# Kernel optimization log

Measured on AMD Instinct MI355X. Metric: run time of the kernel, lower is better.

## Reference

```python
import jax, jax.numpy as jnp
import numpy as np

BB_MIN = -2.0
BB_MAX = 2.0
GRID_RES = 256
VOXEL_SIZE = (BB_MAX - BB_MIN) / (GRID_RES - 1)
# corner order matches torch code x1..x8: (dx,dy,dz) with dx outer, dz inner
CORNERS = [(dx, dy, dz) for dx in (0, 1) for dy in (0, 1) for dz in (0, 1)]


def _grid_normals(g, vs):
    # central differences interior, one-sided extrapolated boundary (as in get_grid_normal)
    def axis_normal(ax):
        n = g.shape[ax] - 1
        sl = lambda a, b: jax.lax.slice_in_dim(g, a, b, axis=ax)
        hi = (3 * sl(n, n + 1) - sl(n - 2, n - 1)) / 2
        lo = (3 * sl(0, 1) - sl(2, 3)) / 2
        fwd = jnp.concatenate([sl(1, n + 1), hi], axis=ax)
        bwd = jnp.concatenate([lo, sl(0, n)], axis=ax)
        return (fwd - bwd) / (2 * vs)
    return axis_normal(0), axis_normal(1), axis_normal(2)


def _gather8(gn, x, y, z):
    # flat index = z + R*y + R*R*x, 8 voxel corners -> [H, W, 8]
    flat = gn.reshape(-1)
    idx = jnp.stack([(z + dz) + GRID_RES * (y + dy) + GRID_RES * GRID_RES * (x + dx)
                     for dx, dy, dz in CORNERS], axis=-1)
    return jnp.take(flat, idx)


def _trilinear(c, tx, ty, tz):
    # weight order matches get_intersection_normal
    w = jnp.stack([
        (1 - tz) * (1 - ty) * (1 - tx), tz * (1 - ty) * (1 - tx),
        (1 - tz) * ty * (1 - tx),       tz * ty * (1 - tx),
        (1 - tz) * (1 - ty) * tx,       tz * (1 - ty) * tx,
        (1 - tz) * ty * tx,             tz * ty * tx], axis=-1)
    return jnp.sum(c * w, axis=-1)


def setup_inputs() -> dict:
    key = jax.random.key(0)
    k0, k1, k2, k3 = jax.random.split(key, 4)
    H, W = 400, 3200
    grid = jax.random.normal(k0, (GRID_RES, GRID_RES, GRID_RES), dtype=jnp.float32) * 0.1
    voxel_idx = jax.random.randint(k1, (H, W, 3), 0, GRID_RES - 1)  # <=254, +1 stays in-range
    voxel_min_point = BB_MIN + voxel_idx.astype(jnp.float32) * VOXEL_SIZE
    intersection_pos = voxel_min_point + jax.random.uniform(k2, (H, W, 3), dtype=jnp.float32) * VOXEL_SIZE
    mask = jax.random.randint(k3, (H, W), 0, 2)
    return {"grid": grid, "voxel_idx": voxel_idx, "intersection_pos": intersection_pos,
            "voxel_min_point": voxel_min_point, "mask": mask}


def reference(grid, voxel_idx, intersection_pos, voxel_min_point, mask):
    nx, ny, nz = _grid_normals(grid, VOXEL_SIZE)
    x = voxel_idx[..., 0]
    y = voxel_idx[..., 1]
    z = voxel_idx[..., 2]
    m = mask.astype(grid.dtype)
    t = (intersection_pos - voxel_min_point) / VOXEL_SIZE
    tx, ty, tz = t[..., 0], t[..., 1], t[..., 2]
    inv = (1 - m)[..., None]  # masked-out rays get +1 on all 8 corners (as in source)
    normals = jnp.stack([
        _trilinear(_gather8(gn, x, y, z) + inv, tx, ty, tz)
        for gn in (nx, ny, nz)], axis=-1)  # [H, W, 3]
    # relu(-grid) value gather at the base corner, zeroed where mask==0
    gridx = jnp.take(jax.nn.relu(-grid).reshape(-1),
                     z + GRID_RES * y + GRID_RES * GRID_RES * x) * m
    return jnp.concatenate([normals, gridx[..., None]], axis=-1)  # [H, W, 4]
```

## Files before the change

kernel.cpp:

```cpp
#include <hip/hip_runtime.h>
#include <hip/hip_bf16.h>

#define GRID_R   256
#define GRID_RR  65536
#define NVOX     16777216
#define NBRK     128
#define INV_2VS  31.875f
#define INV_VS   63.75f
#define VSF      0.015686275f

__device__ __forceinline__ float h2f(unsigned short u) {
    union { unsigned short s; _Float16 f; } cv; cv.s = u; return (float)cv.f;
}
__device__ __forceinline__ unsigned f2h2(float a, float b) {
    union { unsigned short s; _Float16 f; } ca, cb;
    ca.f = (_Float16)a; cb.f = (_Float16)b;
    return (unsigned)ca.s | ((unsigned)cb.s << 16);
}


__global__ __launch_bounds__(256) void precompute_brick_kernel(
    const float* __restrict__ grid,
    uint2*       __restrict__ packed)
{
    int bid = blockIdx.x;
    int t   = threadIdx.x;
    int xcd = bid & 7;
    int idx = bid >> 3;
    int bxl = idx >> 6;
    int byp = idx & 63;
    int bx  = (xcd << 4) + bxl;
    int by  = (byp << 1) + (t >> 7);
    int bz  = t & 127;

    int x0 = bx << 1, y0 = by << 1, z0 = bz << 1;
    int x1 = x0 + 1, y1 = y0 + 1, z1 = z0 + 1;

    int xm = (x0 == 0) ? 0 : x0 - 1;          int xp = (x1 == 255) ? 255 : x1 + 1;
    int ym = (y0 == 0) ? 0 : y0 - 1;          int yp = (y1 == 255) ? 255 : y1 + 1;
    int zm = (z0 == 0) ? 0 : z0 - 1;          int zp = (z1 == 255) ? 255 : z1 + 1;

    #define G2(X,Y,Z) (*reinterpret_cast<const float2*>(grid + (((X)*GRID_R + (Y)) << 8) + (Z)))
    #define G1(X,Y,Z) (grid[(((X)*GRID_R + (Y)) << 8) + (Z)])

    float2 c00 = G2(x0, y0, z0), c01 = G2(x0, y1, z0);
    float2 c10 = G2(x1, y0, z0), c11 = G2(x1, y1, z0);
    float c[2][2][2] = {{{c00.x, c00.y}, {c01.x, c01.y}},
                        {{c10.x, c10.y}, {c11.x, c11.y}}};

    float2 xl0 = G2(xm, y0, z0), xl1 = G2(xm, y1, z0);
    float2 xh0 = G2(xp, y0, z0), xh1 = G2(xp, y1, z0);
    float xlo[2][2] = {{xl0.x, xl0.y}, {xl1.x, xl1.y}};
    float xhi[2][2] = {{xh0.x, xh0.y}, {xh1.x, xh1.y}};

    float2 yl0 = G2(x0, ym, z0), yl1 = G2(x1, ym, z0);
    float2 yh0 = G2(x0, yp, z0), yh1 = G2(x1, yp, z0);
    float ylo[2][2] = {{yl0.x, yl0.y}, {yl1.x, yl1.y}};
    float yhi[2][2] = {{yh0.x, yh0.y}, {yh1.x, yh1.y}};

    float zlo[2][2], zhi[2][2];
    zlo[0][0] = G1(x0, y0, zm); zlo[0][1] = G1(x0, y1, zm);
    zlo[1][0] = G1(x1, y0, zm); zlo[1][1] = G1(x1, y1, zm);
    zhi[0][0] = G1(x0, y0, zp); zhi[0][1] = G1(x0, y1, zp);
    zhi[1][0] = G1(x1, y0, zp); zhi[1][1] = G1(x1, y1, zp);
    #undef G2
    #undef G1

    bool xb0 = (x0 == 0), xb1 = (x1 == 255);
    bool yb0 = (y0 == 0), yb1 = (y1 == 255);
    bool zb0 = (z0 == 0), zb1 = (z1 == 255);

    uint2 slot[8];
    #pragma unroll
    for (int dx = 0; dx < 2; ++dx)
    #pragma unroll
    for (int dy = 0; dy < 2; ++dy)
    #pragma unroll
    for (int dz = 0; dz < 2; ++dz) {
        float g0 = c[dx][dy][dz];

        float nx;
        if (xb0 && dx == 0)      nx = (c[1][dy][dz] - 1.5f*g0 + 0.5f*xhi[dy][dz]) * INV_2VS;
        else if (xb1 && dx == 1) nx = (1.5f*g0 - 0.5f*xlo[dy][dz] - c[0][dy][dz]) * INV_2VS;
        else nx = ((dx ? xhi[dy][dz] : c[1][dy][dz]) - (dx ? c[0][dy][dz] : xlo[dy][dz])) * INV_2VS;

        float ny;
        if (yb0 && dy == 0)      ny = (c[dx][1][dz] - 1.5f*g0 + 0.5f*yhi[dx][dz]) * INV_2VS;
        else if (yb1 && dy == 1) ny = (1.5f*g0 - 0.5f*ylo[dx][dz] - c[dx][0][dz]) * INV_2VS;
        else ny = ((dy ? yhi[dx][dz] : c[dx][1][dz]) - (dy ? c[dx][0][dz] : ylo[dx][dz])) * INV_2VS;

        float nz;
        if (zb0 && dz == 0)      nz = (c[dx][dy][1] - 1.5f*g0 + 0.5f*zhi[dx][dy]) * INV_2VS;
        else if (zb1 && dz == 1) nz = (1.5f*g0 - 0.5f*zlo[dx][dy] - c[dx][dy][0]) * INV_2VS;
        else nz = ((dz ? zhi[dx][dy] : c[dx][dy][1]) - (dz ? c[dx][dy][0] : zlo[dx][dy])) * INV_2VS;

        int s = dx*4 + dy*2 + dz;
        slot[s].x = f2h2(nx, ny);
        slot[s].y = f2h2(nz, g0);
    }

    long long B = ((long long)(bx*NBRK + by))*NBRK + bz;
    uint4* dst = reinterpret_cast<uint4*>(packed) + B*4;
    #pragma unroll
    for (int j = 0; j < 4; ++j) {
        uint4 st; st.x = slot[2*j].x; st.y = slot[2*j].y;
                  st.z = slot[2*j+1].x; st.w = slot[2*j+1].y;
        dst[j] = st;
    }
}

__global__ __launch_bounds__(256) void gather_kernel(
    const uint2* __restrict__ packed,
    const int*   __restrict__ vidx,
    const float* __restrict__ ipos,
    const int*   __restrict__ mask,
    float*       __restrict__ out,
    int n)
{
    int i = blockIdx.x * blockDim.x + threadIdx.x;
    if (i >= n) return;

    int x = vidx[3*i+0];
    int y = vidx[3*i+1];
    int z = vidx[3*i+2];

    float tx = (ipos[3*i+0] - (-2.0f + (float)x * VSF)) * INV_VS;
    float ty = (ipos[3*i+1] - (-2.0f + (float)y * VSF)) * INV_VS;
    float tz = (ipos[3*i+2] - (-2.0f + (float)z * VSF)) * INV_VS;

    int   m   = mask[i];
    float inv = 1.0f - (float)m;

    float ox = 1.0f - tx, oy = 1.0f - ty, oz = 1.0f - tz;
    float w[8];
    w[0] = oz*oy*ox;  w[1] = tz*oy*ox;  w[2] = oz*ty*ox;  w[3] = tz*ty*ox;
    w[4] = oz*oy*tx;  w[5] = tz*oy*tx;  w[6] = oz*ty*tx;  w[7] = tz*ty*tx;

    float accx = 0.f, accy = 0.f, accz = 0.f;
    float gbase = 0.f;

    #pragma unroll
    for (int k = 0; k < 8; ++k) {
        int cx = x + (k >> 2), cy = y + ((k >> 1) & 1), cz = z + (k & 1);
        int B  = ((cx >> 1)*NBRK + (cy >> 1))*NBRK + (cz >> 1);
        int s  = (cx & 1)*4 + (cy & 1)*2 + (cz & 1);
        uint2 p = packed[B*8 + s];
        accx += h2f(p.x & 0xffff) * w[k];
        accy += h2f(p.x >> 16)    * w[k];
        accz += h2f(p.y & 0xffff) * w[k];
        if (k == 0) gbase = h2f(p.y >> 16);
    }

    float4 o;
    o.x = accx + inv;
    o.y = accy + inv;
    o.z = accz + inv;
    o.w = fmaxf(-gbase, 0.0f) * (float)m;
    *reinterpret_cast<float4*>(out + 4*i) = o;
}

__global__ __launch_bounds__(256) void sdf_grid_kernel(
    const float* __restrict__ grid,
    const int*   __restrict__ vidx,
    const float* __restrict__ ipos,
    const float* __restrict__ vmin,
    const int*   __restrict__ mask,
    float*       __restrict__ out,
    int n)
{
    int i = blockIdx.x * blockDim.x + threadIdx.x;
    if (i >= n) return;
    int x = vidx[3*i+0], y = vidx[3*i+1], z = vidx[3*i+2];
    float tx = (ipos[3*i+0] - vmin[3*i+0]) * INV_VS;
    float ty = (ipos[3*i+1] - vmin[3*i+1]) * INV_VS;
    float tz = (ipos[3*i+2] - vmin[3*i+2]) * INV_VS;
    int   m   = mask[i];
    float inv = 1.0f - (float)m;
    float ox = 1.0f - tx, oy = 1.0f - ty, oz = 1.0f - tz;
    float w[8];
    w[0] = oz*oy*ox;  w[1] = tz*oy*ox;  w[2] = oz*ty*ox;  w[3] = tz*ty*ox;
    w[4] = oz*oy*tx;  w[5] = tz*oy*tx;  w[6] = oz*ty*tx;  w[7] = tz*ty*tx;
    int base = z + GRID_R*y + GRID_RR*x;
    float nout[3];
    #pragma unroll
    for (int a = 0; a < 3; ++a) {
        const int s  = (a==0) ? GRID_RR : (a==1) ? GRID_R : 1;
        const int c0 = (a==0) ? x : (a==1) ? y : z;
        float acc = 0.0f;
        #pragma unroll
        for (int k = 0; k < 8; ++k) {
            const int dx = k>>2, dy = (k>>1)&1, dz = k&1;
            const int b  = base + dz + GRID_R*dy + GRID_RR*dx;
            const int cc = c0 + ((a==0) ? dx : (a==1) ? dy : dz);
            float v;
            if (cc == 0)            v = grid[b+s] - (3.0f*grid[b] - grid[b+2*s])*0.5f;
            else if (cc == GRID_R-1) v = (3.0f*grid[b] - grid[b-2*s])*0.5f - grid[b-s];
            else                    v = grid[b+s] - grid[b-s];
            acc += (v*INV_2VS + inv) * w[k];
        }
        nout[a] = acc;
    }
    float gx = fmaxf(-grid[base], 0.0f) * (float)m;
    float4 o; o.x = nout[0]; o.y = nout[1]; o.z = nout[2]; o.w = gx;
    *reinterpret_cast<float4*>(out + 4*i) = o;
}

extern "C" void kernel_launch(void* const* d_in, const int* in_sizes, int n_in,
                              void* d_out, int out_size, void* d_ws, size_t ws_size,
                              hipStream_t stream) {
    const float* grid = (const float*)d_in[0];
    const int*   vidx = (const int*)d_in[1];
    const float* ipos = (const float*)d_in[2];
    const float* vmin = (const float*)d_in[3];
    const int*   mask = (const int*)d_in[4];
    float*       out  = (float*)d_out;

    const int n = in_sizes[4];
    const int block = 256;

    if (ws_size >= (size_t)NVOX * 8) {
        uint2* packed = (uint2*)d_ws;
        precompute_brick_kernel<<<8192, block, 0, stream>>>(grid, packed);
        gather_kernel<<<(n + block - 1) / block, block, 0, stream>>>(
            packed, vidx, ipos, mask, out, n);
    } else {
        sdf_grid_kernel<<<(n + block - 1) / block, block, 0, stream>>>(
            grid, vidx, ipos, vmin, mask, out, n);
    }
}
```

Baseline: 257.7 us.

## Stage grid tiles with halo in LDS for brick normal precompute

```diff
diff --git a/kernel.cpp b/kernel.cpp
--- a/kernel.cpp
+++ b/kernel.cpp
@@ -19,56 +19,67 @@
 }
 
 
-__global__ __launch_bounds__(256) void precompute_brick_kernel(
+__global__ __launch_bounds__(256) void precompute_tile_kernel(
     const float* __restrict__ grid,
     uint2*       __restrict__ packed)
 {
-    int bid = blockIdx.x;
-    int t   = threadIdx.x;
-    int xcd = bid & 7;
-    int idx = bid >> 3;
-    int bxl = idx >> 6;
-    int byp = idx & 63;
-    int bx  = (xcd << 4) + bxl;
-    int by  = (byp << 1) + (t >> 7);
-    int bz  = t & 127;
-
-    int x0 = bx << 1, y0 = by << 1, z0 = bz << 1;
-    int x1 = x0 + 1, y1 = y0 + 1, z1 = z0 + 1;
-
-    int xm = (x0 == 0) ? 0 : x0 - 1;          int xp = (x1 == 255) ? 255 : x1 + 1;
-    int ym = (y0 == 0) ? 0 : y0 - 1;          int yp = (y1 == 255) ? 255 : y1 + 1;
-    int zm = (z0 == 0) ? 0 : z0 - 1;          int zp = (z1 == 255) ? 255 : z1 + 1;
-
-    #define G2(X,Y,Z) (*reinterpret_cast<const float2*>(grid + (((X)*GRID_R + (Y)) << 8) + (Z)))
-    #define G1(X,Y,Z) (grid[(((X)*GRID_R + (Y)) << 8) + (Z)])
-
-    float2 c00 = G2(x0, y0, z0), c01 = G2(x0, y1, z0);
-    float2 c10 = G2(x1, y0, z0), c11 = G2(x1, y1, z0);
-    float c[2][2][2] = {{{c00.x, c00.y}, {c01.x, c01.y}},
-                        {{c10.x, c10.y}, {c11.x, c11.y}}};
-
-    float2 xl0 = G2(xm, y0, z0), xl1 = G2(xm, y1, z0);
-    float2 xh0 = G2(xp, y0, z0), xh1 = G2(xp, y1, z0);
-    float xlo[2][2] = {{xl0.x, xl0.y}, {xl1.x, xl1.y}};
-    float xhi[2][2] = {{xh0.x, xh0.y}, {xh1.x, xh1.y}};
-
-    float2 yl0 = G2(x0, ym, z0), yl1 = G2(x1, ym, z0);
-    float2 yh0 = G2(x0, yp, z0), yh1 = G2(x1, yp, z0);
-    float ylo[2][2] = {{yl0.x, yl0.y}, {yl1.x, yl1.y}};
-    float yhi[2][2] = {{yh0.x, yh0.y}, {yh1.x, yh1.y}};
-
-    float zlo[2][2], zhi[2][2];
-    zlo[0][0] = G1(x0, y0, zm); zlo[0][1] = G1(x0, y1, zm);
-    zlo[1][0] = G1(x1, y0, zm); zlo[1][1] = G1(x1, y1, zm);
-    zhi[0][0] = G1(x0, y0, zp); zhi[0][1] = G1(x0, y1, zp);
-    zhi[1][0] = G1(x1, y0, zp); zhi[1][1] = G1(x1, y1, zp);
-    #undef G2
-    #undef G1
-
-    bool xb0 = (x0 == 0), xb1 = (x1 == 255);
-    bool yb0 = (y0 == 0), yb1 = (y1 == 255);
-    bool zb0 = (z0 == 0), zb1 = (z1 == 255);
+    __shared__ float ls[10*10*40];
+    __shared__ uint4 lout[256*4];
+
+    const int bid = blockIdx.x;
+    const int t   = threadIdx.x;
+    const int tz  = bid & 7;
+    const int ty  = (bid >> 3) & 31;
+    const int tx  = bid >> 8;
+    const int xt0 = tx << 3, yt0 = ty << 3, zt0 = tz << 5;
+
+    #pragma unroll
+    for (int it = 0; it < 4; ++it) {
+        int w = t + (it << 8);
+        if (w < 1000) {
+            int lx  = w / 100;
+            int rem = w - lx * 100;
+            int ly  = rem / 10;
+            int seg = rem - ly * 10;
+            int gx = min(max(xt0 - 1 + lx, 0), 255);
+            int gy = min(max(yt0 - 1 + ly, 0), 255);
+            int zb = min(max(zt0 - 4 + (seg << 2), 0), 252);
+            float4 v = *reinterpret_cast<const float4*>(
+                grid + (gx << 16) + (gy << 8) + zb);
+            *reinterpret_cast<float4*>(&ls[(lx * 10 + ly) * 40 + (seg << 2)]) = v;
+        }
+    }
+    __syncthreads();
+
+    const int lbz = t & 15, lby = (t >> 4) & 3, lbx = t >> 6;
+    const int Lx = lbx << 1, Ly = lby << 1, Lz = lbz << 1;
+    #define S(ix,iy,iz) ls[((1 + Lx + (ix)) * 10 + (1 + Ly + (iy))) * 40 + (4 + Lz + (iz))]
+
+    float c[2][2][2], xlo[2][2], xhi[2][2], ylo[2][2], yhi[2][2], zlo[2][2], zhi[2][2];
+    #pragma unroll
+    for (int dy = 0; dy < 2; ++dy)
+    #pragma unroll
+    for (int dz = 0; dz < 2; ++dz) { xlo[dy][dz] = S(-1, dy, dz); xhi[dy][dz] = S(2, dy, dz); }
+    #pragma unroll
+    for (int dx = 0; dx < 2; ++dx)
+    #pragma unroll
+    for (int dz = 0; dz < 2; ++dz) { ylo[dx][dz] = S(dx, -1, dz); yhi[dx][dz] = S(dx, 2, dz); }
+    #pragma unroll
+    for (int dx = 0; dx < 2; ++dx)
+    #pragma unroll
+    for (int dy = 0; dy < 2; ++dy) { zlo[dx][dy] = S(dx, dy, -1); zhi[dx][dy] = S(dx, dy, 2); }
+    #pragma unroll
+    for (int dx = 0; dx < 2; ++dx)
+    #pragma unroll
+    for (int dy = 0; dy < 2; ++dy)
+    #pragma unroll
+    for (int dz = 0; dz < 2; ++dz) c[dx][dy][dz] = S(dx, dy, dz);
+    #undef S
+
+    const int x0 = xt0 + Lx, y0 = yt0 + Ly, z0 = zt0 + Lz;
+    const bool xb0 = (x0 == 0), xb1 = (x0 + 1 == 255);
+    const bool yb0 = (y0 == 0), yb1 = (y0 + 1 == 255);
+    const bool zb0 = (z0 == 0), zb1 = (z0 + 1 == 255);
 
     uint2 slot[8];
     #pragma unroll
@@ -99,14 +110,24 @@
         slot[s].y = f2h2(nz, g0);
     }
 
-    long long B = ((long long)(bx*NBRK + by))*NBRK + bz;
-    uint4* dst = reinterpret_cast<uint4*>(packed) + B*4;
     #pragma unroll
     for (int j = 0; j < 4; ++j) {
-        uint4 st; st.x = slot[2*j].x; st.y = slot[2*j].y;
+        uint4 st; st.x = slot[2*j].x;   st.y = slot[2*j].y;
                   st.z = slot[2*j+1].x; st.w = slot[2*j+1].y;
-        dst[j] = st;
-    }
+        lout[t*4 + j] = st;
+    }
+    __syncthreads();
+
+    const int chunk = t >> 4;
+    const int idx   = t & 15;
+    const int cbx = (tx << 2) + (chunk >> 2);
+    const int cby = (ty << 2) + (chunk & 3);
+    const long long Bg = ((long long)(cbx * NBRK + cby)) * NBRK + (tz << 4);
+    uint4*       gdst = reinterpret_cast<uint4*>(packed) + Bg * 4;
+    const uint4* lsrc = &lout[chunk << 6];
+    #pragma unroll
+    for (int j = 0; j < 4; ++j)
+        gdst[idx + (j << 4)] = lsrc[idx + (j << 4)];
 }
 
 __global__ __launch_bounds__(256) void gather_kernel(
@@ -220,7 +241,7 @@
 
     if (ws_size >= (size_t)NVOX * 8) {
         uint2* packed = (uint2*)d_ws;
-        precompute_brick_kernel<<<8192, block, 0, stream>>>(grid, packed);
+        precompute_tile_kernel<<<8192, block, 0, stream>>>(grid, packed);
         gather_kernel<<<(n + block - 1) / block, block, 0, stream>>>(
             packed, vidx, ipos, mask, out, n);
     } else {
```

Result: faster. 235.7 us (-8.5%).
